# Kernel optimization log

Hardware: AMD Instinct MI355X
Metric: run time of the kernel (lower is better)

## Reference

```python
import jax, jax.numpy as jnp
import numpy as np

B, T, D, H = 4, 2048, 1024, 16
HS = D // H  # head_size = 64
EPS = 1e-5


def _layernorm(x, g, b):
    mu = jnp.mean(x, axis=-1, keepdims=True)
    var = jnp.var(x, axis=-1, keepdims=True)
    return (x - mu) * jax.lax.rsqrt(var + EPS) * g + b


def setup_inputs() -> dict:
    key = jax.random.key(0)
    ks = jax.random.split(key, 12)
    s = lambda fan_in: 1.0 / np.sqrt(fan_in)
    return {
        "x": jax.random.normal(ks[0], (B, T, D), dtype=jnp.float32),
        # per-head projections, stacked: (H, D, HS)
        "Wq": jax.random.uniform(ks[1], (H, D, HS), jnp.float32, -s(D), s(D)),
        "Wk": jax.random.uniform(ks[2], (H, D, HS), jnp.float32, -s(D), s(D)),
        "Wv": jax.random.uniform(ks[3], (H, D, HS), jnp.float32, -s(D), s(D)),
        "Wo": jax.random.uniform(ks[4], (D, D), jnp.float32, -s(D), s(D)),
        "bo": jax.random.uniform(ks[5], (D,), jnp.float32, -s(D), s(D)),
        "W1": jax.random.uniform(ks[6], (D, 4 * D), jnp.float32, -s(D), s(D)),
        "b1": jax.random.uniform(ks[7], (4 * D,), jnp.float32, -s(D), s(D)),
        "W2": jax.random.uniform(ks[8], (4 * D, D), jnp.float32, -s(4 * D), s(4 * D)),
        "b2": jax.random.uniform(ks[9], (D,), jnp.float32, -s(4 * D), s(4 * D)),
        "g1": jnp.ones((D,), jnp.float32),
        "be1": jnp.zeros((D,), jnp.float32),
        "g2": jnp.ones((D,), jnp.float32),
        "be2": jnp.zeros((D,), jnp.float32),
    }


def reference(x, Wq, Wk, Wv, Wo, bo, W1, b1, W2, b2, g1, be1, g2, be2):
    # --- self-attention sublayer (pre-LN) ---
    h = _layernorm(x, g1, be1)                       # (B,T,D)
    q = jnp.einsum('btd,hds->bhts', h, Wq)           # (B,H,T,HS)
    k = jnp.einsum('btd,hds->bhts', h, Wk)
    v = jnp.einsum('btd,hds->bhts', h, Wv)
    scores = jnp.einsum('bhts,bhus->bhtu', q, k) * (HS ** -0.5)  # (B,H,T,T)
    causal = jnp.tril(jnp.ones((T, T), dtype=bool))
    scores = jnp.where(causal, scores, -jnp.inf)
    w = jax.nn.softmax(scores, axis=-1)
    attn = jnp.einsum('bhtu,bhus->bhts', w, v)       # (B,H,T,HS)
    attn = attn.transpose(0, 2, 1, 3).reshape(B, T, D)  # concat heads
    x = x + attn @ Wo + bo
    # --- feed-forward sublayer (pre-LN) ---
    h2 = _layernorm(x, g2, be2)
    x = x + jax.nn.relu(h2 @ W1 + b1) @ W2 + b2
    return x
```

## Files before the change

### kernel.cpp

```cpp
#include <hip/hip_runtime.h>
#include <hip/hip_bf16.h>
#include <cstddef>

#define B_ 4
#define T_ 2048
#define D_ 1024
#define H_ 16
#define HS_ 64
#define QKS_ 2048

typedef short short8 __attribute__((ext_vector_type(8)));
typedef float f32x4 __attribute__((ext_vector_type(4)));

__device__ __forceinline__ unsigned short f2b(float x) {
    __hip_bfloat16 b = __float2bfloat16(x);
    return *reinterpret_cast<unsigned short*>(&b);
}

__device__ __forceinline__ void gload_lds16(const void* g, void* l) {
    __builtin_amdgcn_global_load_lds((const __attribute__((address_space(1))) void*)g,
                                     (__attribute__((address_space(3))) void*)l, 16, 0, 0);
}

__global__ __launch_bounds__(256) void ln_kernel(const float* __restrict__ X,
                                                 const float* __restrict__ g,
                                                 const float* __restrict__ be,
                                                 unsigned short* __restrict__ O)
{
    const int row = blockIdx.x;
    const int tid = threadIdx.x;
    const float* xr = X + (size_t)row * D_;
    float4 xv = *reinterpret_cast<const float4*>(xr + tid * 4);
    float s  = xv.x + xv.y + xv.z + xv.w;
    float s2 = xv.x * xv.x + xv.y * xv.y + xv.z * xv.z + xv.w * xv.w;
#pragma unroll
    for (int off = 32; off > 0; off >>= 1) {
        s  += __shfl_xor(s,  off);
        s2 += __shfl_xor(s2, off);
    }
    __shared__ float red[8];
    const int wid = tid >> 6, lane = tid & 63;
    if (lane == 0) { red[wid * 2] = s; red[wid * 2 + 1] = s2; }
    __syncthreads();
    s  = red[0] + red[2] + red[4] + red[6];
    s2 = red[1] + red[3] + red[5] + red[7];
    const float mu  = s * (1.0f / D_);
    const float var = s2 * (1.0f / D_) - mu * mu;
    const float r   = rsqrtf(var + 1e-5f);
    float4 gv = *reinterpret_cast<const float4*>(g  + tid * 4);
    float4 bv = *reinterpret_cast<const float4*>(be + tid * 4);
    ushort4 ov;
    ov.x = f2b((xv.x - mu) * r * gv.x + bv.x);
    ov.y = f2b((xv.y - mu) * r * gv.y + bv.y);
    ov.z = f2b((xv.z - mu) * r * gv.z + bv.z);
    ov.w = f2b((xv.w - mu) * r * gv.w + bv.w);
    *reinterpret_cast<ushort4*>(O + (size_t)row * D_ + tid * 4) = ov;
}

__global__ __launch_bounds__(256) void transpose_all(const float* __restrict__ Wq,
                                                     const float* __restrict__ Wk,
                                                     const float* __restrict__ Wv,
                                                     const float* __restrict__ Wo,
                                                     const float* __restrict__ W1,
                                                     const float* __restrict__ W2,
                                                     unsigned short* __restrict__ Wtqkv,
                                                     unsigned short* __restrict__ Wto,
                                                     unsigned short* __restrict__ Wt1,
                                                     unsigned short* __restrict__ Wt2)
{
    __shared__ float tile[32][33];
    const int tx = threadIdx.x & 31, ty = threadIdx.x >> 5;
    int s = blockIdx.x;

    if (s < 3072) {
        const float* in = (s < 1024) ? Wq : (s < 2048) ? Wk : Wv;
        const int noff = (s < 1024) ? 0 : (s < 2048) ? D_ : 2 * D_;
        s &= 1023;
        const int bn = (s & 31) * 32, bk = (s >> 5) * 32;
        const int head = bn >> 6, s0 = bn & 63;
#pragma unroll
        for (int i = 0; i < 32; i += 8)
            tile[ty + i][tx] = in[(size_t)head * D_ * HS_ + (size_t)(bk + ty + i) * HS_ + s0 + tx];
        __syncthreads();
#pragma unroll
        for (int i = 0; i < 32; i += 8)
            Wtqkv[(size_t)(noff + bn + ty + i) * D_ + bk + tx] = f2b(tile[tx][ty + i]);
        return;
    }
    s -= 3072;
    const float* in; unsigned short* out; int K, N, bn, bk;
    if (s < 1024)      { in = Wo; out = Wto; K = D_;     N = D_;     bn = (s & 31) * 32;  bk = (s >> 5) * 32; }
    else if (s < 5120) { s -= 1024; in = W1; out = Wt1; K = D_;     N = 4 * D_; bn = (s & 127) * 32; bk = (s >> 7) * 32; }
    else               { s -= 5120; in = W2; out = Wt2; K = 4 * D_; N = D_;     bn = (s & 31) * 32;  bk = (s >> 5) * 32; }
#pragma unroll
    for (int i = 0; i < 32; i += 8)
        tile[ty + i][tx] = in[(size_t)(bk + ty + i) * N + bn + tx];
    __syncthreads();
#pragma unroll
    for (int i = 0; i < 32; i += 8)
        out[(size_t)(bn + ty + i) * K + bk + tx] = f2b(tile[tx][ty + i]);
}

template<bool BIAS, bool RELU, bool RESID, bool OUT_BF16, bool SCALEQ>
__global__ __launch_bounds__(512, 1) void gemm_sq(const unsigned short* __restrict__ A,
                                                  const unsigned short* __restrict__ Bt,
                                                  const float* __restrict__ bias,
                                                  const float* __restrict__ resid,
                                                  float* __restrict__ Cf,
                                                  unsigned short* __restrict__ Cb,
                                                  int M, int N, int K)
{
    constexpr int BUFS = 16384 + 16384;
    __shared__ __attribute__((aligned(128))) unsigned short lds[2 * BUFS];

    const int tid = threadIdx.x, l = tid & 63, w = tid >> 6;
    const int wRow = w >> 2, wCol = w & 3;
    const int lr = l & 15, lq = l >> 4;

    const int gx = gridDim.x;
    const int nwg = gx * (int)gridDim.y;
    const int orig = (int)blockIdx.y * gx + (int)blockIdx.x;
    const int xcd = orig & 7, lo = orig >> 3;
    const int q8 = nwg >> 3, r8 = nwg & 7;
    const int wg = (xcd < r8 ? xcd * (q8 + 1) : r8 * (q8 + 1) + (xcd - r8) * q8) + lo;
    const int bm = wg / gx, bn = wg % gx;

    const int nt = K >> 6;

    auto ISSUE_HALF = [&](int t, int half) {
        const size_t kof = (size_t)t * 64;
        const int buf = t & 1;
        const unsigned short* src = (half < 2) ? A : Bt;
        const int rb = ((half < 2) ? bm : bn) * 256 + (half & 1) * 128;
        const int lb = buf * BUFS + ((half >= 2) ? 16384 : 0) + (half & 1) * 128 * 64;
#pragma unroll
        for (int p = 0; p < 2; ++p) {
            const int j = p * 512 + tid;
            const int row = j >> 3, ci = j & 7;
            gload_lds16(src + (size_t)(rb + row) * K + kof + ((ci ^ (row & 7)) * 8),
                        &lds[lb + j * 8]);
        }
    };

    f32x4 acc[8][4];
#pragma unroll
    for (int i = 0; i < 8; ++i)
#pragma unroll
        for (int j = 0; j < 4; ++j) acc[i][j] = (f32x4){0.f, 0.f, 0.f, 0.f};

    short8 af[4][2], bf[4][2];
    const int swz = lr & 7;

#pragma unroll
    for (int h = 0; h < 4; ++h) ISSUE_HALF(0, h);

    for (int t = 0; t < nt; ++t) {
        const unsigned short* As = &lds[(t & 1) * BUFS];
        const unsigned short* Bs = As + 16384;
        const bool more = (t + 1 < nt);

        asm volatile("s_waitcnt vmcnt(0)" ::: "memory");
        __builtin_amdgcn_s_barrier();

        if (more) ISSUE_HALF(t + 1, 0);
#pragma unroll
        for (int mi = 0; mi < 4; ++mi) {
            const int row = wRow * 128 + mi * 16 + lr;
#pragma unroll
            for (int ks = 0; ks < 2; ++ks)
                af[mi][ks] = *reinterpret_cast<const short8*>(&As[row * 64 + (((ks * 4 + lq) ^ swz) * 8)]);
        }
#pragma unroll
        for (int nj = 0; nj < 2; ++nj) {
            const int rowB = wCol * 64 + nj * 16 + lr;
#pragma unroll
            for (int ks = 0; ks < 2; ++ks)
                bf[nj][ks] = *reinterpret_cast<const short8*>(&Bs[rowB * 64 + (((ks * 4 + lq) ^ swz) * 8)]);
        }
        asm volatile("s_waitcnt lgkmcnt(0)" ::: "memory");
        __builtin_amdgcn_sched_barrier(0);
        __builtin_amdgcn_s_setprio(1);
#pragma unroll
        for (int mi = 0; mi < 4; ++mi)
#pragma unroll
            for (int nj = 0; nj < 2; ++nj)
#pragma unroll
                for (int ks = 0; ks < 2; ++ks)
                    acc[mi][nj] = __builtin_amdgcn_mfma_f32_16x16x32_bf16(af[mi][ks], bf[nj][ks], acc[mi][nj], 0, 0, 0);
        __builtin_amdgcn_s_setprio(0);

        if (more) ISSUE_HALF(t + 1, 1);
#pragma unroll
        for (int nj = 2; nj < 4; ++nj) {
            const int rowB = wCol * 64 + nj * 16 + lr;
#pragma unroll
            for (int ks = 0; ks < 2; ++ks)
                bf[nj][ks] = *reinterpret_cast<const short8*>(&Bs[rowB * 64 + (((ks * 4 + lq) ^ swz) * 8)]);
        }
        asm volatile("s_waitcnt lgkmcnt(0)" ::: "memory");
        __builtin_amdgcn_sched_barrier(0);
        __builtin_amdgcn_s_setprio(1);
#pragma unroll
        for (int mi = 0; mi < 4; ++mi)
#pragma unroll
            for (int nj = 2; nj < 4; ++nj)
#pragma unroll
                for (int ks = 0; ks < 2; ++ks)
                    acc[mi][nj] = __builtin_amdgcn_mfma_f32_16x16x32_bf16(af[mi][ks], bf[nj][ks], acc[mi][nj], 0, 0, 0);
        __builtin_amdgcn_s_setprio(0);

        if (more) { ISSUE_HALF(t + 1, 2); ISSUE_HALF(t + 1, 3); }
#pragma unroll
        for (int mi = 0; mi < 4; ++mi) {
            const int row = wRow * 128 + (4 + mi) * 16 + lr;
#pragma unroll
            for (int ks = 0; ks < 2; ++ks)
                af[mi][ks] = *reinterpret_cast<const short8*>(&As[row * 64 + (((ks * 4 + lq) ^ swz) * 8)]);
        }
        asm volatile("s_waitcnt lgkmcnt(0)" ::: "memory");
        __builtin_amdgcn_sched_barrier(0);
        __builtin_amdgcn_s_setprio(1);
#pragma unroll
        for (int mi = 0; mi < 4; ++mi)
#pragma unroll
            for (int nj = 0; nj < 2; ++nj)
#pragma unroll
                for (int ks = 0; ks < 2; ++ks)
                    acc[4 + mi][nj] = __builtin_amdgcn_mfma_f32_16x16x32_bf16(af[mi][ks], bf[nj][ks], acc[4 + mi][nj], 0, 0, 0);
        __builtin_amdgcn_s_setprio(0);

        __builtin_amdgcn_s_setprio(1);
#pragma unroll
        for (int mi = 0; mi < 4; ++mi)
#pragma unroll
            for (int nj = 2; nj < 4; ++nj)
#pragma unroll
                for (int ks = 0; ks < 2; ++ks)
                    acc[4 + mi][nj] = __builtin_amdgcn_mfma_f32_16x16x32_bf16(af[mi][ks], bf[nj][ks], acc[4 + mi][nj], 0, 0, 0);
        __builtin_amdgcn_s_setprio(0);
    }

    const int m0 = bm * 256 + wRow * 128;
    const int n0 = bn * 256 + wCol * 64;
    if constexpr (OUT_BF16) {
        __syncthreads();
        unsigned short* ldsE = lds + w * 8192;
#pragma unroll
        for (int nf = 0; nf < 4; ++nf) {
            const int col = n0 + nf * 16 + lr;
            const float bv = BIAS ? bias[col] : 0.0f;
#pragma unroll
            for (int mf = 0; mf < 8; ++mf) {
#pragma unroll
                for (int r = 0; r < 4; ++r) {
                    float c = acc[mf][nf][r] + bv;
                    if (RELU) c = fmaxf(c, 0.0f);
                    if (SCALEQ) { if (col < D_) c *= 0.18033688f; }
                    ldsE[(mf * 16 + lq * 4 + r) * 64 + nf * 16 + lr] = f2b(c);
                }
            }
        }
        asm volatile("s_waitcnt lgkmcnt(0)" ::: "memory");
        const int lg = l >> 3, lc = (l & 7) * 8;
#pragma unroll
        for (int i = 0; i < 16; ++i) {
            const int rowl = i * 8 + lg;
            short8 v = *reinterpret_cast<const short8*>(&ldsE[rowl * 64 + lc]);
            *reinterpret_cast<short8*>(&Cb[(size_t)(m0 + rowl) * N + n0 + lc]) = v;
        }
    } else {
#pragma unroll
        for (int nf = 0; nf < 4; ++nf) {
            const int col = n0 + nf * 16 + lr;
            const float bv = BIAS ? bias[col] : 0.0f;
#pragma unroll
            for (int mf = 0; mf < 8; ++mf) {
#pragma unroll
                for (int r = 0; r < 4; ++r) {
                    const int row = m0 + mf * 16 + lq * 4 + r;
                    float c = acc[mf][nf][r] + bv;
                    if (RELU) c = fmaxf(c, 0.0f);
                    if (RESID) c += resid[(size_t)row * N + col];
                    if (SCALEQ) { if (col < D_) c *= 0.18033688f; }
                    Cf[(size_t)row * N + col] = c;
                }
            }
        }
    }
}

template<bool BIAS, bool RELU, bool RESID, bool OUT_BF16, bool SCALEQ, bool VONLY>
__global__ __launch_bounds__(512, 1) void gemm_sq2(const unsigned short* __restrict__ A,
                                                   const unsigned short* __restrict__ Bt,
                                                   const float* __restrict__ bias,
                                                   const float* __restrict__ resid,
                                                   float* __restrict__ Cf,
                                                   unsigned short* __restrict__ Cb,
                                                   unsigned short* __restrict__ Vt,
                                                   int M, int N, int K)
{
    constexpr int BUFS = 8192 + 16384;
    __shared__ __attribute__((aligned(128))) unsigned short lds[3 * BUFS];

    const int tid = threadIdx.x, l = tid & 63, w = tid >> 6;
    const int wRow = w >> 2, wCol = w & 3;
    const int lr = l & 15, lq = l >> 4;

    const int gx = gridDim.x;
    const int nwg = gx * (int)gridDim.y;
    const int orig = (int)blockIdx.y * gx + (int)blockIdx.x;
    const int xcd = orig & 7, lo = orig >> 3;
    const int q8 = nwg >> 3, r8 = nwg & 7;
    const int wg = (xcd < r8 ? xcd * (q8 + 1) : r8 * (q8 + 1) + (xcd - r8) * q8) + lo;
    const int bm = wg / gx, bn = wg % gx;

    const int nt = K >> 6;

    auto ISSUE = [&](int t, int buf) {
        const size_t kof = (size_t)t * 64;
#pragma unroll
        for (int p = 0; p < 2; ++p) {
            const int j = p * 512 + tid;
            const int row = j >> 3, ci = j & 7;
            gload_lds16(A + (size_t)(bm * 128 + row) * K + kof + ((ci ^ (row & 7)) * 8),
                        &lds[buf * BUFS + j * 8]);
        }
#pragma unroll
        for (int p = 0; p < 4; ++p) {
            const int j = p * 512 + tid;
            const int row = j >> 3, ci = j & 7;
            gload_lds16(Bt + (size_t)(bn * 256 + row) * K + kof + ((ci ^ (row & 7)) * 8),
                        &lds[buf * BUFS + 8192 + j * 8]);
        }
    };

    f32x4 acc[4][4];
#pragma unroll
    for (int i = 0; i < 4; ++i)
#pragma unroll
        for (int j = 0; j < 4; ++j) acc[i][j] = (f32x4){0.f, 0.f, 0.f, 0.f};

    short8 af[2][2], bf[4][2];
    const int swz = lr & 7;

    ISSUE(0, 0);
    ISSUE(1, 1);

    for (int t = 0; t < nt; ++t) {
        const unsigned short* As = &lds[(t % 3) * BUFS];
        const unsigned short* Bs = As + 8192;
        if (t + 1 < nt) asm volatile("s_waitcnt vmcnt(6)" ::: "memory");
        else            asm volatile("s_waitcnt vmcnt(0)" ::: "memory");
        __builtin_amdgcn_s_barrier();
        if (t + 2 < nt) ISSUE(t + 2, (t + 2) % 3);

#pragma unroll
        for (int mi = 0; mi < 2; ++mi) {
            const int row = wRow * 64 + mi * 16 + lr;
#pragma unroll
            for (int ks = 0; ks < 2; ++ks)
                af[mi][ks] = *reinterpret_cast<const short8*>(&As[row * 64 + (((ks * 4 + lq) ^ swz) * 8)]);
        }
#pragma unroll
        for (int nj = 0; nj < 4; ++nj) {
            const int rowB = wCol * 64 + nj * 16 + lr;
#pragma unroll
            for (int ks = 0; ks < 2; ++ks)
                bf[nj][ks] = *reinterpret_cast<const short8*>(&Bs[rowB * 64 + (((ks * 4 + lq) ^ swz) * 8)]);
        }
        asm volatile("s_waitcnt lgkmcnt(0)" ::: "memory");
        __builtin_amdgcn_sched_barrier(0);
        __builtin_amdgcn_s_setprio(1);
#pragma unroll
        for (int mi = 0; mi < 2; ++mi)
#pragma unroll
            for (int nj = 0; nj < 4; ++nj)
#pragma unroll
                for (int ks = 0; ks < 2; ++ks)
                    acc[mi][nj] = __builtin_amdgcn_mfma_f32_16x16x32_bf16(af[mi][ks], bf[nj][ks], acc[mi][nj], 0, 0, 0);
        __builtin_amdgcn_s_setprio(0);

#pragma unroll
        for (int mi = 0; mi < 2; ++mi) {
            const int row = wRow * 64 + (2 + mi) * 16 + lr;
#pragma unroll
            for (int ks = 0; ks < 2; ++ks)
                af[mi][ks] = *reinterpret_cast<const short8*>(&As[row * 64 + (((ks * 4 + lq) ^ swz) * 8)]);
        }
        asm volatile("s_waitcnt lgkmcnt(0)" ::: "memory");
        __builtin_amdgcn_sched_barrier(0);
        __builtin_amdgcn_s_setprio(1);
#pragma unroll
        for (int mi = 0; mi < 2; ++mi)
#pragma unroll
            for (int nj = 0; nj < 4; ++nj)
#pragma unroll
                for (int ks = 0; ks < 2; ++ks)
                    acc[2 + mi][nj] = __builtin_amdgcn_mfma_f32_16x16x32_bf16(af[mi][ks], bf[nj][ks], acc[2 + mi][nj], 0, 0, 0);
        __builtin_amdgcn_s_setprio(0);
    }

    if (VONLY) {
        __syncthreads();
        unsigned short* ldsT = lds;
        const int n0l = wCol * 64;
        const int m0l = wRow * 64;
#pragma unroll
        for (int nf = 0; nf < 4; ++nf) {
            const int cl = n0l + nf * 16 + lr;
#pragma unroll
            for (int mf = 0; mf < 4; ++mf) {
#pragma unroll
                for (int r = 0; r < 4; ++r) {
                    const int rl = m0l + mf * 16 + lq * 4 + r;
                    const int pos = (rl & 64) + (((rl & 15) << 2) | ((rl >> 4) & 3));
                    ldsT[cl * 136 + pos] = f2b(acc[mf][nf][r]);
                }
            }
        }
        __syncthreads();
        const int rowT = tid >> 1, half = tid & 1;
        const int colV = bn * 256 + rowT;
        const int hd = colV >> 6, sdim = colV & 63;
        const int bb = bm >> 4;
        const int tt0 = (bm & 15) * 128 + half * 64;
        unsigned short* dst = Vt + (((size_t)(bb * H_ + hd) * 64 + sdim) << 11) + tt0;
        const unsigned short* srcl = &ldsT[rowT * 136 + half * 64];
#pragma unroll
        for (int i = 0; i < 8; ++i)
            *reinterpret_cast<short8*>(dst + i * 8) =
                *reinterpret_cast<const short8*>(srcl + i * 8);
        return;
    }

    const int m0 = bm * 128 + wRow * 64;
    const int n0 = bn * 256 + wCol * 64;
#pragma unroll
    for (int nf = 0; nf < 4; ++nf) {
        const int col = n0 + nf * 16 + lr;
        const float bv = BIAS ? bias[col] : 0.0f;
#pragma unroll
        for (int mf = 0; mf < 4; ++mf) {
#pragma unroll
            for (int r = 0; r < 4; ++r) {
                const int row = m0 + mf * 16 + lq * 4 + r;
                float c = acc[mf][nf][r] + bv;
                if (RELU) c = fmaxf(c, 0.0f);
                if (RESID) c += resid[(size_t)row * N + col];
                if (SCALEQ) { if (col < D_) c *= 0.18033688f; }
                if (OUT_BF16) Cb[(size_t)row * N + col] = f2b(c);
                else          Cf[(size_t)row * N + col] = c;
            }
        }
    }
}

template<bool MASKED>
__device__ __forceinline__ void attn_chunk(
    const unsigned short* __restrict__ ksb,
    const unsigned short* __restrict__ vsb,
    unsigned short (* __restrict__ psw)[72],
    const short8* aq, f32x4* o,
    int lr, int lq, int wl)
{
    const short8 vone = {0x3F80, 0x3F80, 0x3F80, 0x3F80, 0x3F80, 0x3F80, 0x3F80, 0x3F80};
    f32x4 s[4];
#pragma unroll
    for (int kb = 0; kb < 4; ++kb) s[kb] = (f32x4){0.f, 0.f, 0.f, 0.f};
    __builtin_amdgcn_s_setprio(1);
#pragma unroll
    for (int kb = 0; kb < 4; ++kb) {
        if (MASKED && kb > wl) continue;
        const int row = kb * 16 + lr;
        const int sw = row & 7;
#pragma unroll
        for (int ks = 0; ks < 2; ++ks) {
            const int ch = (ks * 4 + lq) ^ sw;
            const short8 bk = *reinterpret_cast<const short8*>(&ksb[row * 64 + ch * 8]);
            s[kb] = __builtin_amdgcn_mfma_f32_16x16x32_bf16(aq[ks], bk, s[kb], 0, 0, 0);
        }
    }
    __builtin_amdgcn_s_setprio(0);

#pragma unroll
    for (int r = 0; r < 4; ++r) {
        const int qloc = wl * 16 + lq * 4 + r;
        float p[4];
#pragma unroll
        for (int kb = 0; kb < 4; ++kb) {
            const bool msk = MASKED && (kb * 16 + lr > qloc);
            p[kb] = msk ? 0.0f : exp2f(s[kb][r]);
        }
        const unsigned int w0 = (unsigned int)f2b(p[0]) | ((unsigned int)f2b(p[1]) << 16);
        const unsigned int w1 = (unsigned int)f2b(p[2]) | ((unsigned int)f2b(p[3]) << 16);
        uint2 pk; pk.x = w0; pk.y = w1;
        *reinterpret_cast<uint2*>(&psw[lq * 4 + r][lr * 4]) = pk;
    }
    asm volatile("s_waitcnt lgkmcnt(0)" ::: "memory");
    __builtin_amdgcn_s_setprio(1);
#pragma unroll
    for (int ks = 0; ks < 2; ++ks) {
        const short8 pa = *reinterpret_cast<const short8*>(&psw[lr][ks * 32 + lq * 8]);
#pragma unroll
        for (int df = 0; df < 4; ++df) {
            const int vrow = df * 16 + lr;
            const int vch = (ks * 4 + lq) ^ (vrow & 7);
            const short8 vb = *reinterpret_cast<const short8*>(&vsb[vrow * 64 + vch * 8]);
            o[df] = __builtin_amdgcn_mfma_f32_16x16x32_bf16(pa, vb, o[df], 0, 0, 0);
        }
        o[4] = __builtin_amdgcn_mfma_f32_16x16x32_bf16(pa, vone, o[4], 0, 0, 0);
    }
    __builtin_amdgcn_s_setprio(0);
}

__global__ __launch_bounds__(512, 4) void attn_mfma(const unsigned short* __restrict__ QK,
                                                    const unsigned short* __restrict__ Vt,
                                                    unsigned short* __restrict__ Og)
{
    __shared__ __attribute__((aligned(128))) unsigned short Ks[2][64 * 64];
    __shared__ __attribute__((aligned(128))) unsigned short Vs[2][64 * 64];
    __shared__ __attribute__((aligned(16)))  unsigned short Ps[8][16][72];

    const int NQT = T_ / 128;
    const int px = blockIdx.x;
    const int qtA = px, qtB = NQT - 1 - px;
    const int h = blockIdx.y, b = blockIdx.z;
    const int tid = threadIdx.x, w = tid >> 6, l = tid & 63;
    const int wl = w & 3, qsub = w >> 2;
    const int lr = l & 15, lq = l >> 4;
    const size_t base = (size_t)b * T_ * QKS_ + h * HS_;

    short8 aqA[2], aqB[2];
    {
        const int qrl = qsub * 64 + wl * 16 + lr;
        const unsigned short* pA = QK + base + (size_t)(qtA * 128 + qrl) * QKS_;
        const unsigned short* pB = QK + base + (size_t)(qtB * 128 + qrl) * QKS_;
        aqA[0] = *reinterpret_cast<const short8*>(pA + lq * 8);
        aqA[1] = *reinterpret_cast<const short8*>(pA + 32 + lq * 8);
        aqB[0] = *reinterpret_cast<const short8*>(pB + lq * 8);
        aqB[1] = *reinterpret_cast<const short8*>(pB + 32 + lq * 8);
    }

    const unsigned short* Kg = QK + D_;
    const unsigned short* Vg = Vt + ((size_t)(b * H_ + h) * 64 << 11);

    auto stage = [&](int c, int bf) {
        const int kbase = c * 64;
        const int row = tid >> 3;
        const int cx = ((tid & 7) ^ (row & 7)) * 8;
        gload_lds16(Kg + base + (size_t)(kbase + row) * QKS_ + cx, &Ks[bf][tid * 8]);
        gload_lds16(Vg + ((size_t)row << 11) + kbase + cx, &Vs[bf][tid * 8]);
    };

    stage(0, 0);
    __syncthreads();

    unsigned short (*psw)[72] = Ps[w];

    f32x4 oA[5], oB[5];
#pragma unroll
    for (int df = 0; df < 5; ++df) {
        oA[df] = (f32x4){0.f, 0.f, 0.f, 0.f};
        oB[df] = (f32x4){0.f, 0.f, 0.f, 0.f};
    }

    const int qminw = qsub * 64 + wl * 16;
    const int qmaxw = qminw + 15;

    const int nch = 2 * qtB + 2;
    int bf = 0;
    for (int c = 0; c < nch; ++c) {
        if (c + 1 < nch) stage(c + 1, bf ^ 1);
        const int relA = c * 64 - qtA * 128;
        const int relB = c * 64 - qtB * 128;
        if (relA <= qmaxw) {
            if (relA + 63 <= qminw)
                attn_chunk<false>(&Ks[bf][0], &Vs[bf][0], psw, aqA, oA, lr, lq, wl);
            else
                attn_chunk<true>(&Ks[bf][0], &Vs[bf][0], psw, aqA, oA, lr, lq, wl);
        }
        if (relB <= qmaxw) {
            if (relB + 63 <= qminw)
                attn_chunk<false>(&Ks[bf][0], &Vs[bf][0], psw, aqB, oB, lr, lq, wl);
            else
                attn_chunk<true>(&Ks[bf][0], &Vs[bf][0], psw, aqB, oB, lr, lq, wl);
        }
        if (c + 1 < nch) __syncthreads();
        bf ^= 1;
    }

    const size_t obase = (size_t)b * T_ * D_ + h * HS_;
#pragma unroll
    for (int r = 0; r < 4; ++r) {
        const float invA = 1.0f / oA[4][r];
        const float invB = 1.0f / oB[4][r];
        const int qrl = qsub * 64 + wl * 16 + lq * 4 + r;
        unsigned short* orowA = Og + obase + (size_t)(qtA * 128 + qrl) * D_;
        unsigned short* orowB = Og + obase + (size_t)(qtB * 128 + qrl) * D_;
#pragma unroll
        for (int df = 0; df < 4; ++df) {
            orowA[df * 16 + lr] = f2b(oA[df][r] * invA);
            orowB[df * 16 + lr] = f2b(oB[df][r] * invB);
        }
    }
}

extern "C" void kernel_launch(void* const* d_in, const int* in_sizes, int n_in,
                              void* d_out, int out_size, void* d_ws, size_t ws_size,
                              hipStream_t stream)
{
    const float* x   = (const float*)d_in[0];
    const float* Wq  = (const float*)d_in[1];
    const float* Wk  = (const float*)d_in[2];
    const float* Wv  = (const float*)d_in[3];
    const float* Wo  = (const float*)d_in[4];
    const float* bo  = (const float*)d_in[5];
    const float* W1  = (const float*)d_in[6];
    const float* b1  = (const float*)d_in[7];
    const float* W2  = (const float*)d_in[8];
    const float* b2  = (const float*)d_in[9];
    const float* g1  = (const float*)d_in[10];
    const float* be1 = (const float*)d_in[11];
    const float* g2  = (const float*)d_in[12];
    const float* be2 = (const float*)d_in[13];
    float* out = (float*)d_out;

    unsigned short* ws = (unsigned short*)d_ws;
    const size_t NT = (size_t)B_ * T_;
    unsigned short* hb    = ws;
    unsigned short* QKb   = hb + NT * D_;
    unsigned short* Ab    = QKb + NT * 3 * D_;
    unsigned short* f1    = QKb;
    unsigned short* Wtqkv = Ab + NT * D_;
    unsigned short* Wto   = Wtqkv + (size_t)3 * D_ * D_;
    unsigned short* Wt1   = Wto + (size_t)D_ * D_;
    unsigned short* Wt2   = Wt1 + (size_t)4 * D_ * D_;
    unsigned short* Vtb   = Wt2 + (size_t)4 * D_ * D_;

    dim3 b256(256), b512(512);

    transpose_all<<<dim3(12288), b256, 0, stream>>>(Wq, Wk, Wv, Wo, W1, W2,
                                                    Wtqkv, Wto, Wt1, Wt2);

    ln_kernel<<<NT, b256, 0, stream>>>(x, g1, be1, hb);

    gemm_sq<false, false, false, true, true><<<dim3(2 * D_ / 256, NT / 256), b512, 0, stream>>>(
        hb, Wtqkv, nullptr, nullptr, nullptr, QKb, (int)NT, 2 * D_, D_);

    gemm_sq2<false, false, false, false, false, true><<<dim3(D_ / 256, NT / 128), b512, 0, stream>>>(
        hb, Wtqkv + (size_t)2 * D_ * D_, nullptr, nullptr, nullptr, nullptr, Vtb, (int)NT, D_, D_);

    attn_mfma<<<dim3(T_ / 256, H_, B_), b512, 0, stream>>>(QKb, Vtb, Ab);

    gemm_sq2<true, false, true, false, false, false><<<dim3(D_ / 256, NT / 128), b512, 0, stream>>>(
        Ab, Wto, bo, x, out, nullptr, nullptr, (int)NT, D_, D_);

    ln_kernel<<<NT, b256, 0, stream>>>(out, g2, be2, hb);

    gemm_sq<true, true, false, true, false><<<dim3(4 * D_ / 256, NT / 256), b512, 0, stream>>>(
        hb, Wt1, b1, nullptr, nullptr, f1, (int)NT, 4 * D_, D_);

    gemm_sq2<true, false, true, false, false, false><<<dim3(D_ / 256, NT / 128), b512, 0, stream>>>(
        f1, Wt2, b2, out, out, nullptr, nullptr, (int)NT, D_, 4 * D_);
}
```

Measured before the change: 325.4 us.

## Halve GEMM K-tile to 32 to fit two workgroups per CU

The bf16 GEMM now stages 32-wide K slices instead of 64, which halves the triple-buffered LDS footprint. Launch bounds move to two 512-thread blocks per CU. The global-to-LDS swizzle, wait counts and fragment loads are rewritten for the narrower tile, and the two-phase MFMA loop becomes a single 4x4 phase per step. The aim is more resident waves to hide latency, at the cost of twice as many barriers and loop iterations and a tighter register budget.

```diff
diff --git a/kernel.cpp b/kernel.cpp
--- a/kernel.cpp
+++ b/kernel.cpp
@@ -290,7 +290,7 @@
 }
 
 template<bool BIAS, bool RELU, bool RESID, bool OUT_BF16, bool SCALEQ, bool VONLY>
-__global__ __launch_bounds__(512, 1) void gemm_sq2(const unsigned short* __restrict__ A,
+__global__ __launch_bounds__(512, 2) void gemm_sq2(const unsigned short* __restrict__ A,
                                                    const unsigned short* __restrict__ Bt,
                                                    const float* __restrict__ bias,
                                                    const float* __restrict__ resid,
@@ -299,7 +299,7 @@
                                                    unsigned short* __restrict__ Vt,
                                                    int M, int N, int K)
 {
-    constexpr int BUFS = 8192 + 16384;
+    constexpr int BUFS = 4096 + 8192;
     __shared__ __attribute__((aligned(128))) unsigned short lds[3 * BUFS];
 
     const int tid = threadIdx.x, l = tid & 63, w = tid >> 6;
@@ -314,23 +314,21 @@
     const int wg = (xcd < r8 ? xcd * (q8 + 1) : r8 * (q8 + 1) + (xcd - r8) * q8) + lo;
     const int bm = wg / gx, bn = wg % gx;
 
-    const int nt = K >> 6;
+    const int nt = K >> 5;
 
     auto ISSUE = [&](int t, int buf) {
-        const size_t kof = (size_t)t * 64;
+        const size_t kof = (size_t)t * 32;
+        {
+            const int row = tid >> 2, ci = tid & 3;
+            gload_lds16(A + (size_t)(bm * 128 + row) * K + kof + ((ci ^ ((row >> 1) & 3)) * 8),
+                        &lds[buf * BUFS + tid * 8]);
+        }
 #pragma unroll
         for (int p = 0; p < 2; ++p) {
             const int j = p * 512 + tid;
-            const int row = j >> 3, ci = j & 7;
-            gload_lds16(A + (size_t)(bm * 128 + row) * K + kof + ((ci ^ (row & 7)) * 8),
-                        &lds[buf * BUFS + j * 8]);
-        }
-#pragma unroll
-        for (int p = 0; p < 4; ++p) {
-            const int j = p * 512 + tid;
-            const int row = j >> 3, ci = j & 7;
-            gload_lds16(Bt + (size_t)(bn * 256 + row) * K + kof + ((ci ^ (row & 7)) * 8),
-                        &lds[buf * BUFS + 8192 + j * 8]);
+            const int row = j >> 2, ci = j & 3;
+            gload_lds16(Bt + (size_t)(bn * 256 + row) * K + kof + ((ci ^ ((row >> 1) & 3)) * 8),
+                        &lds[buf * BUFS + 4096 + j * 8]);
         }
     };
 
@@ -340,63 +338,37 @@
 #pragma unroll
         for (int j = 0; j < 4; ++j) acc[i][j] = (f32x4){0.f, 0.f, 0.f, 0.f};
 
-    short8 af[2][2], bf[4][2];
-    const int swz = lr & 7;
+    short8 af[4], bf[4];
 
     ISSUE(0, 0);
-    ISSUE(1, 1);
+    if (nt > 1) ISSUE(1, 1);
 
     for (int t = 0; t < nt; ++t) {
         const unsigned short* As = &lds[(t % 3) * BUFS];
-        const unsigned short* Bs = As + 8192;
-        if (t + 1 < nt) asm volatile("s_waitcnt vmcnt(6)" ::: "memory");
+        const unsigned short* Bs = As + 4096;
+        if (t + 1 < nt) asm volatile("s_waitcnt vmcnt(3)" ::: "memory");
         else            asm volatile("s_waitcnt vmcnt(0)" ::: "memory");
         __builtin_amdgcn_s_barrier();
         if (t + 2 < nt) ISSUE(t + 2, (t + 2) % 3);
 
 #pragma unroll
-        for (int mi = 0; mi < 2; ++mi) {
+        for (int mi = 0; mi < 4; ++mi) {
             const int row = wRow * 64 + mi * 16 + lr;
-#pragma unroll
-            for (int ks = 0; ks < 2; ++ks)
-                af[mi][ks] = *reinterpret_cast<const short8*>(&As[row * 64 + (((ks * 4 + lq) ^ swz) * 8)]);
+            af[mi] = *reinterpret_cast<const short8*>(&As[row * 32 + ((lq ^ ((row >> 1) & 3)) * 8)]);
         }
 #pragma unroll
         for (int nj = 0; nj < 4; ++nj) {
             const int rowB = wCol * 64 + nj * 16 + lr;
-#pragma unroll
-            for (int ks = 0; ks < 2; ++ks)
-                bf[nj][ks] = *reinterpret_cast<const short8*>(&Bs[rowB * 64 + (((ks * 4 + lq) ^ swz) * 8)]);
+            bf[nj] = *reinterpret_cast<const short8*>(&Bs[rowB * 32 + ((lq ^ ((rowB >> 1) & 3)) * 8)]);
         }
         asm volatile("s_waitcnt lgkmcnt(0)" ::: "memory");
         __builtin_amdgcn_sched_barrier(0);
         __builtin_amdgcn_s_setprio(1);
 #pragma unroll
-        for (int mi = 0; mi < 2; ++mi)
+        for (int mi = 0; mi < 4; ++mi)
 #pragma unroll
             for (int nj = 0; nj < 4; ++nj)
-#pragma unroll
-                for (int ks = 0; ks < 2; ++ks)
-                    acc[mi][nj] = __builtin_amdgcn_mfma_f32_16x16x32_bf16(af[mi][ks], bf[nj][ks], acc[mi][nj], 0, 0, 0);
-        __builtin_amdgcn_s_setprio(0);
-
-#pragma unroll
-        for (int mi = 0; mi < 2; ++mi) {
-            const int row = wRow * 64 + (2 + mi) * 16 + lr;
-#pragma unroll
-            for (int ks = 0; ks < 2; ++ks)
-                af[mi][ks] = *reinterpret_cast<const short8*>(&As[row * 64 + (((ks * 4 + lq) ^ swz) * 8)]);
-        }
-        asm volatile("s_waitcnt lgkmcnt(0)" ::: "memory");
-        __builtin_amdgcn_sched_barrier(0);
-        __builtin_amdgcn_s_setprio(1);
-#pragma unroll
-        for (int mi = 0; mi < 2; ++mi)
-#pragma unroll
-            for (int nj = 0; nj < 4; ++nj)
-#pragma unroll
-                for (int ks = 0; ks < 2; ++ks)
-                    acc[2 + mi][nj] = __builtin_amdgcn_mfma_f32_16x16x32_bf16(af[mi][ks], bf[nj][ks], acc[2 + mi][nj], 0, 0, 0);
+                acc[mi][nj] = __builtin_amdgcn_mfma_f32_16x16x32_bf16(af[mi], bf[nj], acc[mi][nj], 0, 0, 0);
         __builtin_amdgcn_s_setprio(0);
     }
 
```

New measurement: 346.0 us. 6.3% more time.
